# Performance work log

Hardware: AMD Instinct MI355X
Metric: run time of the kernel (lower is better)

Reference implementation:

```python
import jax, jax.numpy as jnp
import numpy as np

IMG = 640.0
NC = 20
LAMBDA_BOX, LAMBDA_OBJ, LAMBDA_CLS = 0.05, 1.0, 0.5
ANCHORS = jnp.array([[10,13],[16,30],[33,23],[30,61],[62,45],[59,119],[116,90],[156,198],[373,326]], dtype=jnp.float32) / IMG
SCALES = [(80,80),(40,40),(20,20)]


def build_target(boxes, labels, scale_idx):
    # boxes: (N,M,4) [x1,y1,x2,y2] in pixels; labels: (N,M) int
    H, W = SCALES[scale_idx]
    anc = ANCHORS[scale_idx*3:(scale_idx+1)*3]            # (3,2)
    N, M, _ = boxes.shape
    x1, y1, x2, y2 = boxes[...,0], boxes[...,1], boxes[...,2], boxes[...,3]
    valid = (x2 > x1) & (y2 > y1)                          # skip degenerate boxes
    cx = (x1 + x2) / 2.0 / IMG
    cy = (y1 + y2) / 2.0 / IMG
    w  = (x2 - x1) / IMG
    h  = (y2 - y1) / IMG
    gx = jnp.floor(cx * W).astype(jnp.int32)               # int() truncation (coords >=0)
    gy = jnp.floor(cy * H).astype(jnp.int32)
    dx = cx * W - gx
    dy = cy * H - gy
    rw = w[..., None] / anc[:, 0]                          # (N,M,3)
    rh = h[..., None] / anc[:, 1]
    ious = jnp.minimum(rw, 1.0/rw) * jnp.minimum(rh, 1.0/rh)
    best = jnp.argmax(ious, axis=-1)                       # (N,M)
    aw, ah = anc[best, 0], anc[best, 1]
    tw = jnp.log(w / aw + 1e-6)
    th = jnp.log(h / ah + 1e-6)
    onehot = jax.nn.one_hot(labels, NC, dtype=boxes.dtype) # (N,M,NC)
    vec = jnp.concatenate([jnp.stack([dx, dy, tw, th, jnp.ones_like(dx)], axis=-1), onehot], axis=-1)  # (N,M,5+NC)
    # route invalid boxes out of range -> dropped by scatter
    gy_s = jnp.where(valid, gy, -1)
    gx_s = jnp.where(valid, gx, -1)
    b = jnp.broadcast_to(jnp.arange(N)[:, None], (N, M))
    ch = jnp.arange(5 + NC)
    t = jnp.zeros((N, 3, 5 + NC, H, W), boxes.dtype)
    t = t.at[b[..., None], best[..., None], ch[None, None, :], gy_s[..., None], gx_s[..., None]].set(vec, mode='drop')
    return t


def bce_with_logits_mean(x, t):
    return jnp.mean(jnp.maximum(x, 0.0) - x * t + jnp.log1p(jnp.exp(-jnp.abs(x))))


def bbox_iou(b1, b2, eps=1e-7):
    # b1,b2: (...,4) center format [cx,cy,w,h]
    b1x1 = b1[...,0]-b1[...,2]/2; b1y1 = b1[...,1]-b1[...,3]/2
    b1x2 = b1[...,0]+b1[...,2]/2; b1y2 = b1[...,1]+b1[...,3]/2
    b2x1 = b2[...,0]-b2[...,2]/2; b2y1 = b2[...,1]-b2[...,3]/2
    b2x2 = b2[...,0]+b2[...,2]/2; b2y2 = b2[...,1]+b2[...,3]/2
    iw = jnp.clip(jnp.minimum(b1x2, b2x2) - jnp.maximum(b1x1, b2x1), 0.0)
    ih = jnp.clip(jnp.minimum(b1y2, b2y2) - jnp.maximum(b1y1, b2y1), 0.0)
    inter = iw * ih
    union = (b1x2-b1x1)*(b1y2-b1y1) + (b2x2-b2x1)*(b2y2-b2y1) - inter + eps
    return inter / union


def yolo_loss(preds, boxes, labels, scale_idx):
    H, W = SCALES[scale_idx]
    stride = IMG / H
    A = 3
    anc = ANCHORS[scale_idx*A:(scale_idx+1)*A]
    target = build_target(boxes, labels, scale_idx)        # (N,A,5+NC,H,W)
    preds = preds.reshape(-1, A, 5 + NC, H, W)
    p_obj = preds[:, :, 4]
    p_cls = preds[:, :, 5:]
    t_obj = target[:, :, 4]
    t_cls = target[:, :, 5:]
    ygrid, xgrid = jnp.meshgrid(jnp.arange(H), jnp.arange(W), indexing='ij')
    grid = jnp.stack((xgrid, ygrid), 2).reshape(1, 1, H, W, 2).astype(preds.dtype)
    p_txty = jnp.transpose(preds[:, :, 0:2], (0, 1, 3, 4, 2))   # (N,A,H,W,2)
    p_twth = jnp.transpose(preds[:, :, 2:4], (0, 1, 3, 4, 2))
    p_xy = (2.0 * jax.nn.sigmoid(p_txty) - 0.5 + grid) * stride
    p_wh = (2.0 * jax.nn.sigmoid(p_twth)) ** 2 * anc.reshape(1, A, 1, 1, 2)
    p_box = jnp.concatenate([p_xy, p_wh], axis=-1)
    t_txty = jnp.transpose(target[:, :, 0:2], (0, 1, 3, 4, 2))
    t_twth = jnp.transpose(target[:, :, 2:4], (0, 1, 3, 4, 2))
    t_xy = (t_txty + grid) * stride
    t_wh = jnp.exp(t_twth) * anc.reshape(1, A, 1, 1, 2)
    t_box = jnp.concatenate([t_xy, t_wh], axis=-1)
    pos = (t_obj == 1.0).astype(preds.dtype)                   # (N,A,H,W)
    iou_sum = jnp.sum(bbox_iou(p_box, t_box) * pos)
    loss_box = 1.0 - iou_sum
    loss_obj = bce_with_logits_mean(p_obj, t_obj)
    loss_cls = bce_with_logits_mean(p_cls, t_cls)
    return LAMBDA_BOX * loss_box + LAMBDA_OBJ * loss_obj + LAMBDA_CLS * loss_cls


def setup_inputs() -> dict:
    key = jax.random.key(0)
    k1, k2, k3 = jax.random.split(key, 3)
    N, M = 64, 40
    preds = jax.random.normal(k1, (N, 3, 5 + NC, 80, 80), dtype=jnp.float32)
    # sample corner pairs in [0,640) and sort so x1<x2, y1<y2
    xy = jnp.sort(jax.random.uniform(k2, (N, M, 2, 2), minval=0.0, maxval=640.0), axis=-1)
    boxes = jnp.stack([xy[..., 0, 0], xy[..., 1, 0], xy[..., 0, 1], xy[..., 1, 1]], axis=-1)
    labels = jax.random.randint(k3, (N, M), 0, NC, dtype=jnp.int32)
    return {"preds": preds, "boxes": boxes, "labels": labels, "scale_idx": 0}


def reference(preds, boxes, labels, scale_idx):
    return yolo_loss(preds, boxes, labels, scale_idx)
```

## Files before the change

kernel.cpp:

```cpp
#include <hip/hip_runtime.h>
#include <math.h>

namespace {
constexpr int kNImg = 64;
constexpr int kM    = 40;
constexpr int kA    = 3;
constexpr int kNC   = 20;
constexpr int kH    = 80;
constexpr int kW    = 80;
constexpr int kHW   = kH * kW;
constexpr int kHW4  = kHW / 4;
constexpr int kC    = 5 + kNC;
constexpr int kPPF4 = kC * kHW4;
constexpr int kVPP  = (1 + kNC) * kHW4;
constexpr int kNV   = kNImg * kA * kVPP;
constexpr float kInvObjF  = 1.0f / 1228800.0f;
constexpr float kHInvClsF = 0.5f / 24576000.0f;
constexpr int kGrid = 1024;
}

typedef float f4v __attribute__((ext_vector_type(4)));

__device__ __forceinline__ float wave_red(float v) {
#pragma unroll
  for (int o = 32; o > 0; o >>= 1) v += __shfl_down(v, o, 64);
  return v;
}

__device__ __forceinline__ float softplus_fast(float x) {
  return fmaxf(x, 0.0f) + __logf(1.0f + __expf(-fabsf(x)));
}

__global__ __launch_bounds__(256) void yolo_fused(
    const float* __restrict__ preds, const float* __restrict__ boxes,
    const int* __restrict__ labels, float* __restrict__ out, int nblocks) {
  __shared__ int s_keys[64];
  __shared__ float s_red[4];
  const int tid = threadIdx.x;
  const int bid = blockIdx.x;

  float acc = 0.0f;

  const float ancw[3] = {10.0f / 640.0f, 16.0f / 640.0f, 33.0f / 640.0f};
  const float anch[3] = {13.0f / 640.0f, 30.0f / 640.0f, 23.0f / 640.0f};

  int mykey = -1, best = 0, gx = 0, gy = 0, lab = 0;
  float dx = 0.0f, dy = 0.0f, twv = 0.0f, thv = 0.0f;

  if (bid < kNImg && tid < 64) {
    int key = -1;
    if (tid < kM) {
      const float* bp = boxes + ((bid * kM + tid) << 2);
      float x1 = bp[0], y1 = bp[1], x2 = bp[2], y2 = bp[3];
      bool valid = (x2 > x1) && (y2 > y1);
      float cx = ((x1 + x2) * 0.5f) / 640.0f;
      float cy = ((y1 + y2) * 0.5f) / 640.0f;
      float w = (x2 - x1) / 640.0f;
      float h = (y2 - y1) / 640.0f;
      float fx = cx * (float)kW;
      float fy = cy * (float)kH;
      gx = (int)floorf(fx);
      gy = (int)floorf(fy);
      dx = fx - (float)gx;
      dy = fy - (float)gy;
      float bestv = -1e30f;
      int b = 0;
#pragma unroll
      for (int a = 0; a < 3; ++a) {
        float rw = w / ancw[a];
        float rh = h / anch[a];
        float i1 = fminf(rw, 1.0f / rw) * fminf(rh, 1.0f / rh);
        if (i1 > bestv) { bestv = i1; b = a; }
      }
      best = b;
      twv = logf(w / ancw[b] + 1e-6f);
      thv = logf(h / anch[b] + 1e-6f);
      lab = labels[bid * kM + tid];
      if (valid && gx >= 0 && gx < kW && gy >= 0 && gy < kH)
        key = (b * kH + gy) * kW + gx;
    }
    s_keys[tid] = key;
    mykey = key;
  }
  __syncthreads();

  if (mykey >= 0) {
    bool win = true;
    for (int mp = tid + 1; mp < kM; ++mp)
      if (s_keys[mp] == mykey) { win = false; break; }
    if (win) {
      const float* pp =
          preds + (size_t)(bid * kA + best) * kC * kHW + (gy * kW + gx);
      float xtx = pp[0];
      float xty = pp[kHW];
      float xtw = pp[2 * kHW];
      float xth = pp[3 * kHW];
      float xob = pp[4 * kHW];
      float xcl = pp[(5 + lab) * kHW];
      float aw = ancw[best], ah = anch[best];
      float sx = 1.0f / (1.0f + expf(-xtx));
      float sy = 1.0f / (1.0f + expf(-xty));
      float sw = 1.0f / (1.0f + expf(-xtw));
      float sh = 1.0f / (1.0f + expf(-xth));
      float px = (2.0f * sx - 0.5f + (float)gx) * 8.0f;
      float py = (2.0f * sy - 0.5f + (float)gy) * 8.0f;
      float pw = (2.0f * sw) * (2.0f * sw) * aw;
      float ph = (2.0f * sh) * (2.0f * sh) * ah;
      float tx = (dx + (float)gx) * 8.0f;
      float ty = (dy + (float)gy) * 8.0f;
      float tw2 = expf(twv) * aw;
      float th2 = expf(thv) * ah;
      float b1x1 = px - pw * 0.5f, b1x2 = px + pw * 0.5f;
      float b1y1 = py - ph * 0.5f, b1y2 = py + ph * 0.5f;
      float b2x1 = tx - tw2 * 0.5f, b2x2 = tx + tw2 * 0.5f;
      float b2y1 = ty - th2 * 0.5f, b2y2 = ty + th2 * 0.5f;
      float iw = fmaxf(fminf(b1x2, b2x2) - fmaxf(b1x1, b2x1), 0.0f);
      float ih = fmaxf(fminf(b1y2, b2y2) - fmaxf(b1y1, b2y1), 0.0f);
      float inter = iw * ih;
      float uni = (b1x2 - b1x1) * (b1y2 - b1y1) +
                  (b2x2 - b2x1) * (b2y2 - b2y1) - inter + 1e-7f;
      float iou = inter / uni;
      acc = -xob * kInvObjF - xcl * kHInvClsF - 0.05f * iou;
    }
  }

  const f4v* __restrict__ pv = (const f4v*)preds;
  const int stride = nblocks * 256;
  int i = bid * 256 + tid;
  for (; i + stride < kNV; i += 2 * stride) {
    int i1 = i + stride;
    int p0 = i / kVPP, r0 = i - p0 * kVPP;
    int p1 = i1 / kVPP, r1 = i1 - p1 * kVPP;
    f4v v0 = __builtin_nontemporal_load(pv + (p0 * kPPF4 + 4 * kHW4 + r0));
    f4v v1 = __builtin_nontemporal_load(pv + (p1 * kPPF4 + 4 * kHW4 + r1));
    float s0 = softplus_fast(v0.x) + softplus_fast(v0.y) +
               softplus_fast(v0.z) + softplus_fast(v0.w);
    float s1 = softplus_fast(v1.x) + softplus_fast(v1.y) +
               softplus_fast(v1.z) + softplus_fast(v1.w);
    acc = fmaf(s0, (r0 < kHW4) ? kInvObjF : kHInvClsF, acc);
    acc = fmaf(s1, (r1 < kHW4) ? kInvObjF : kHInvClsF, acc);
  }
  if (i < kNV) {
    int p0 = i / kVPP, r0 = i - p0 * kVPP;
    f4v v0 = __builtin_nontemporal_load(pv + (p0 * kPPF4 + 4 * kHW4 + r0));
    float s0 = softplus_fast(v0.x) + softplus_fast(v0.y) +
               softplus_fast(v0.z) + softplus_fast(v0.w);
    acc = fmaf(s0, (r0 < kHW4) ? kInvObjF : kHInvClsF, acc);
  }

  acc = wave_red(acc);
  if ((tid & 63) == 0) s_red[tid >> 6] = acc;
  __syncthreads();
  if (tid == 0) {
    float b = s_red[0] + s_red[1] + s_red[2] + s_red[3];
    if (bid == 0) b += 0.05f;
    atomicAdd(out, b);
  }
}

extern "C" void kernel_launch(void* const* d_in, const int* in_sizes, int n_in,
                              void* d_out, int out_size, void* d_ws,
                              size_t ws_size, hipStream_t stream) {
  const float* preds = (const float*)d_in[0];
  const float* boxes = (const float*)d_in[1];
  const int* labels = (const int*)d_in[2];
  float* out = (float*)d_out;
  (void)d_ws; (void)ws_size;

  yolo_fused<<<kGrid, 256, 0, stream>>>(preds, boxes, labels, out, kGrid);
}
```

Before: 176.0 us.

## Assign each wave one channel plane chunk instead of grid-stride loop

Replaces the grid-stride loop over flattened obj/cls vectors with a fixed mapping where each wave handles one 6400-element channel plane (25 unrolled float4 loads per lane). Per-iteration integer division and the per-element weight select go away, and the weight becomes uniform per wave. The grid becomes 64*3*21/4 = 1008 blocks, each doing exactly one plane chunk, so there is no loop-carried stride. Memory-level parallelism now depends on the unroll of 5 rather than on two independent loads per iteration.

```diff
diff --git a/kernel.cpp b/kernel.cpp
--- a/kernel.cpp
+++ b/kernel.cpp
@@ -12,11 +12,11 @@
 constexpr int kHW4  = kHW / 4;
 constexpr int kC    = 5 + kNC;
 constexpr int kPPF4 = kC * kHW4;
-constexpr int kVPP  = (1 + kNC) * kHW4;
-constexpr int kNV   = kNImg * kA * kVPP;
+constexpr int kChunksPerPlane = 21;
+constexpr int kWavesTotal = kNImg * kA * kChunksPerPlane;
+constexpr int kBlocks = kWavesTotal / 4;
 constexpr float kInvObjF  = 1.0f / 1228800.0f;
 constexpr float kHInvClsF = 0.5f / 24576000.0f;
-constexpr int kGrid = 1024;
 }
 
 typedef float f4v __attribute__((ext_vector_type(4)));
@@ -33,11 +33,13 @@
 
 __global__ __launch_bounds__(256) void yolo_fused(
     const float* __restrict__ preds, const float* __restrict__ boxes,
-    const int* __restrict__ labels, float* __restrict__ out, int nblocks) {
+    const int* __restrict__ labels, float* __restrict__ out) {
   __shared__ int s_keys[64];
   __shared__ float s_red[4];
   const int tid = threadIdx.x;
   const int bid = blockIdx.x;
+  const int lane = tid & 63;
+  const int wid = tid >> 6;
 
   float acc = 0.0f;
 
@@ -124,32 +126,24 @@
     }
   }
 
-  const f4v* __restrict__ pv = (const f4v*)preds;
-  const int stride = nblocks * 256;
-  int i = bid * 256 + tid;
-  for (; i + stride < kNV; i += 2 * stride) {
-    int i1 = i + stride;
-    int p0 = i / kVPP, r0 = i - p0 * kVPP;
-    int p1 = i1 / kVPP, r1 = i1 - p1 * kVPP;
-    f4v v0 = __builtin_nontemporal_load(pv + (p0 * kPPF4 + 4 * kHW4 + r0));
-    f4v v1 = __builtin_nontemporal_load(pv + (p1 * kPPF4 + 4 * kHW4 + r1));
-    float s0 = softplus_fast(v0.x) + softplus_fast(v0.y) +
-               softplus_fast(v0.z) + softplus_fast(v0.w);
-    float s1 = softplus_fast(v1.x) + softplus_fast(v1.y) +
-               softplus_fast(v1.z) + softplus_fast(v1.w);
-    acc = fmaf(s0, (r0 < kHW4) ? kInvObjF : kHInvClsF, acc);
-    acc = fmaf(s1, (r1 < kHW4) ? kInvObjF : kHInvClsF, acc);
-  }
-  if (i < kNV) {
-    int p0 = i / kVPP, r0 = i - p0 * kVPP;
-    f4v v0 = __builtin_nontemporal_load(pv + (p0 * kPPF4 + 4 * kHW4 + r0));
-    float s0 = softplus_fast(v0.x) + softplus_fast(v0.y) +
-               softplus_fast(v0.z) + softplus_fast(v0.w);
-    acc = fmaf(s0, (r0 < kHW4) ? kInvObjF : kHInvClsF, acc);
+  {
+    const int w = bid * 4 + wid;
+    const int plane = w / 21;
+    const int sub = w - plane * 21;
+    const f4v* __restrict__ base =
+        (const f4v*)preds + plane * kPPF4 + 4 * kHW4 + sub * kHW4 + lane;
+    float s = 0.0f;
+#pragma unroll 5
+    for (int it = 0; it < 25; ++it) {
+      f4v v = __builtin_nontemporal_load(base + it * 64);
+      s += softplus_fast(v.x) + softplus_fast(v.y) + softplus_fast(v.z) +
+           softplus_fast(v.w);
+    }
+    acc = fmaf(s, (sub == 0) ? kInvObjF : kHInvClsF, acc);
   }
 
   acc = wave_red(acc);
-  if ((tid & 63) == 0) s_red[tid >> 6] = acc;
+  if (lane == 0) s_red[wid] = acc;
   __syncthreads();
   if (tid == 0) {
     float b = s_red[0] + s_red[1] + s_red[2] + s_red[3];
@@ -167,5 +161,5 @@
   float* out = (float*)d_out;
   (void)d_ws; (void)ws_size;
 
-  yolo_fused<<<kGrid, 256, 0, stream>>>(preds, boxes, labels, out, kGrid);
+  yolo_fused<<<kBlocks, 256, 0, stream>>>(preds, boxes, labels, out);
 }
```

After: 175.2 us. No clear change (-0.5%).
